# Optimization experiments

Measured on AMD Instinct MI355X. Metric: run time of the kernel, lower is better.

The kernel has to match this reference:

```python
import jax, jax.numpy as jnp
import numpy as np

WS = 7          # window size
DIM = 192
HEADS = 6
NW = 64         # number of windows per image (mask leading dim)
NC = 3          # n_contrast (q and kv)
B_ = 1024       # num_windows * batch


def _relative_position_index(ws):
    coords = np.stack(np.meshgrid(np.arange(ws), np.arange(ws), indexing='ij'))  # (2, ws, ws)
    cf = coords.reshape(2, -1)                       # (2, ws*ws)
    rel = cf[:, :, None] - cf[:, None, :]            # (2, N, N)
    rel = rel.transpose(1, 2, 0).copy()              # (N, N, 2)
    rel[:, :, 0] += ws - 1
    rel[:, :, 1] += ws - 1
    rel[:, :, 0] *= 2 * ws - 1
    return rel.sum(-1)                               # (N, N) int

REL_IDX = jnp.asarray(_relative_position_index(WS))


def setup_inputs() -> dict:
    key = jax.random.key(0)
    ks = jax.random.split(key, 13)
    f32 = jnp.float32
    inp = {
        'x_q': jax.random.normal(ks[0], (B_, NC, WS, WS, DIM), f32),
        'x_k': jax.random.normal(ks[1], (B_, NC, WS, WS, DIM), f32),
        'x_v': jax.random.normal(ks[2], (B_, NC, WS, WS, DIM), f32),
        'mask': jax.random.normal(ks[3], (NW, WS * WS, WS * WS), f32),
        # Linear weights stored torch-style: (out_features, in_features)
        'q_w': jax.random.normal(ks[4], (DIM, DIM), f32) * 0.02,
        'q_b': jnp.zeros((DIM,), f32),
        'k_w': jax.random.normal(ks[5], (DIM, DIM), f32) * 0.02,
        'k_b': jnp.zeros((DIM,), f32),
        'v_w': jax.random.normal(ks[6], (DIM, DIM), f32) * 0.02,
        'v_b': jnp.zeros((DIM,), f32),
        'proj_w': jax.random.normal(ks[7], (DIM, DIM), f32) * 0.02,
        'proj_b': jnp.zeros((DIM,), f32),
        'bias_table': jax.random.normal(ks[8], ((2 * WS - 1) ** 2, HEADS), f32) * 0.02,
    }
    return inp


def reference(x_q, x_k, x_v, mask, q_w, q_b, k_w, k_b, v_w, v_b, proj_w, proj_b, bias_table):
    Bw, ncq, Wh, Ww, C = x_q.shape
    nckv = x_k.shape[1]
    H = HEADS
    hd = C // H
    Nq = ncq * Wh * Ww
    Nkv = nckv * Wh * Ww

    xq = x_q.reshape(Bw, Nq, C)
    xk = x_k.reshape(Bw, Nkv, C)
    xv = x_v.reshape(Bw, Nkv, C)

    q = (xq @ q_w.T + q_b).reshape(Bw, Nq, H, hd).transpose(0, 2, 1, 3)   # (B_, H, Nq, hd)
    k = (xk @ k_w.T + k_b).reshape(Bw, Nkv, H, hd).transpose(0, 2, 1, 3)
    v = (xv @ v_w.T + v_b).reshape(Bw, Nkv, H, hd).transpose(0, 2, 1, 3)

    scale = hd ** (-0.5)
    attn = jnp.einsum('bhqd,bhkd->bhqk', q * scale, k)                    # (B_, H, Nq, Nkv)

    Nwin = Wh * Ww
    bias = bias_table[REL_IDX.reshape(-1)].reshape(Nwin, Nwin, H)
    bias = bias.transpose(2, 0, 1)                                        # (H, Nwin, Nwin)
    bias = jnp.tile(bias, (1, ncq, nckv))                                 # (H, Nq, Nkv)
    attn = attn + bias[None]

    nW = mask.shape[0]
    m = jnp.tile(mask, (1, ncq, nckv))                                    # (nW, Nq, Nkv)
    attn = attn.reshape(Bw // nW, nW, H, Nq, Nkv) + m[None, :, None]
    attn = attn.reshape(Bw, H, Nq, Nkv)
    attn = jax.nn.softmax(attn, axis=-1)

    out = jnp.einsum('bhqk,bhkd->bhqd', attn, v)                          # (B_, H, Nq, hd)
    out = out.transpose(0, 2, 1, 3).reshape(Bw, Nq, C)
    out = out @ proj_w.T + proj_b
    return out.reshape(Bw, ncq, Wh, Ww, C)
```

## Files before the change

### kernel.cpp

```cpp
#include <hip/hip_runtime.h>
#include <stdint.h>

#define ROWS 150528
#define QSCALE 0.17677669529663687f
#define L2E 1.44269504088896f

typedef __attribute__((ext_vector_type(8))) __bf16 bf16x8;
typedef __attribute__((ext_vector_type(4))) __bf16 bf16x4;
typedef __attribute__((ext_vector_type(4))) float f32x4;
typedef __attribute__((ext_vector_type(4))) float f4;
typedef __attribute__((ext_vector_type(2))) uint32_t u32x2;

static __device__ __forceinline__ f32x4 mfma_bf16(bf16x8 a, bf16x8 b, f32x4 c) {
  return __builtin_amdgcn_mfma_f32_16x16x32_bf16(a, b, c, 0, 0, 0);
}

static __device__ __forceinline__ uint32_t pack_bf16(float a, float b) {
  uint16_t ux = __builtin_bit_cast(uint16_t, (__bf16)a);
  uint16_t uy = __builtin_bit_cast(uint16_t, (__bf16)b);
  return (uint32_t)ux | ((uint32_t)uy << 16);
}

#define GLOAD_LDS16(gp, lp)                                                     \
  __builtin_amdgcn_global_load_lds(                                             \
      (const __attribute__((address_space(1))) uint32_t*)(gp),                  \
      (__attribute__((address_space(3))) uint32_t*)(lp), 16, 0, 0)

__global__ void prep(const float* __restrict__ q_w, const float* __restrict__ k_w,
                     const float* __restrict__ v_w, const float* __restrict__ p_w,
                     __bf16* __restrict__ wq, __bf16* __restrict__ wk,
                     __bf16* __restrict__ wv, __bf16* __restrict__ wp,
                     const float* __restrict__ maskp, const float* __restrict__ btab,
                     float* __restrict__ bmall) {
  const int bid = blockIdx.x;
  if (bid < 144) {
    const int y = bid / 36;
    const float* s = y == 0 ? q_w : y == 1 ? k_w : y == 2 ? v_w : p_w;
    __bf16* d = y == 0 ? wq : y == 1 ? wk : y == 2 ? wv : wp;
    int i = (bid % 36) * 256 + threadIdx.x;
    f4 v = ((const f4*)s)[i];
    bf16x4 b;
    b[0] = (__bf16)v[0]; b[1] = (__bf16)v[1]; b[2] = (__bf16)v[2]; b[3] = (__bf16)v[3];
    ((bf16x4*)d)[i] = b;
  } else {
    const int idx = bid - 144;
    const int win = idx / 6, h = idx - win * 6;
    float* dst = bmall + ((size_t)idx) * 2800;
    for (int i = threadIdx.x; i < 2796; i += 256) {
      int q = i / 57, ke = i - q * 57;
      int k = ke >= 49 ? ke - 49 : ke;
      if (q > 48) q = 48;
      int qi = q / 7, qj = q - qi * 7, ki = k / 7, kj = k - ki * 7;
      int rel = (qi - ki + 6) * 13 + (qj - kj + 6);
      dst[i] = (maskp[win * 2401 + q * 49 + k] + btab[rel * 6 + h]) * L2E;
    }
  }
}

template<bool IN_F32, bool OUT_F32, int RPT, int TILES>
static __device__ __forceinline__
void gemm_pipe(const void* __restrict__ Xv, const __bf16* __restrict__ Wb,
               const float* __restrict__ bias, void* __restrict__ Ov, float scale,
               char* Xs, int bx)
{
  constexpr int CPR = IN_F32 ? 48 : 24;
  constexpr int LPW = RPT * CPR / 256;
  constexpr int TB  = RPT * CPR * 16;
  constexpr int RG  = RPT / 16;
  constexpr int SPT = RG * 3;
  const int tid = threadIdx.x;
  const int wv = tid >> 6, lane = tid & 63, lr = lane & 15, lg = lane >> 4;
  const size_t blk0 = (size_t)bx * (RPT * TILES);

  bf16x8 wf[3][6];
  f4 bc4[3];
  #pragma unroll
  for (int t = 0; t < 3; ++t) {
    const int nt = wv + 4 * t;
    const __bf16* wr = &Wb[(nt * 16 + lr) * 192 + lg * 8];
    #pragma unroll
    for (int kk = 0; kk < 6; ++kk) wf[t][kk] = *(const bf16x8*)&wr[kk * 32];
    f4 bb = *(const f4*)&bias[nt * 16 + 4 * lg];
    #pragma unroll
    for (int e = 0; e < 4; ++e) bc4[t][e] = bb[e] * scale;
  }

  auto stage = [&](int buf, int t) {
    const size_t row0 = blk0 + (size_t)t * RPT;
    char* ldsb = Xs + buf * TB;
    int l = (wv * LPW) * 64 + lane;
    #pragma unroll
    for (int p = 0; p < LPW; ++p) {
      int r = l / CPR;
      int c16 = (l - r * CPR) ^ (r & 7);
      const char* src;
      if (IN_F32) {
        src = (const char*)Xv + ((row0 + r) * 768 + c16 * 16);
      } else {
        int hh = c16 >> 2, sub = c16 & 3;
        src = (const char*)Xv + (((size_t)hh * ROWS + row0 + r) * 64 + sub * 16);
      }
      GLOAD_LDS16(src, ldsb + (wv * LPW + p) * 1024);
      l += 64;
    }
  };

  stage(0, 0);
  stage(1, 1);

  #pragma unroll
  for (int it = 0; it < TILES; ++it) {
    if (it == 0) {
      asm volatile("s_waitcnt vmcnt(%0)" :: "i"(LPW) : "memory");
    } else if (it == 1) {
      asm volatile("s_waitcnt vmcnt(%0)" :: "i"(SPT + LPW) : "memory");
    } else if (it + 1 < TILES) {
      asm volatile("s_waitcnt vmcnt(%0)" :: "i"(2 * SPT + LPW) : "memory");
    } else {
      asm volatile("s_waitcnt vmcnt(%0)" :: "i"(2 * SPT) : "memory");
    }
    __builtin_amdgcn_s_barrier();

    const size_t row0 = blk0 + (size_t)it * RPT;
    const char* cb = Xs + (it % 3) * TB;

    bf16x8 a[RG][6];
    #pragma unroll
    for (int rg = 0; rg < RG; ++rg) {
      const int rr = rg * 16 + lr;
      const char* rb = cb + rr * (CPR * 16);
      const int sw = rr & 7;
      if (IN_F32) {
        #pragma unroll
        for (int kk = 0; kk < 6; ++kk) {
          const int g0 = kk * 8 + lg * 2;
          f4 lo = *(const f4*)(rb + ((g0 ^ sw) * 16));
          f4 hi = *(const f4*)(rb + (((g0 + 1) ^ sw) * 16));
          #pragma unroll
          for (int e = 0; e < 4; ++e) {
            a[rg][kk][e]     = (__bf16)lo[e];
            a[rg][kk][4 + e] = (__bf16)hi[e];
          }
        }
      } else {
        #pragma unroll
        for (int kk = 0; kk < 6; ++kk) {
          const int g = kk * 4 + lg;
          a[rg][kk] = *(const bf16x8*)(rb + ((g ^ sw) * 16));
        }
      }
    }

    if (it + 2 < TILES) stage((it + 2) % 3, it + 2);
    asm volatile("" ::: "memory");

    #pragma unroll
    for (int rg = 0; rg < RG; ++rg) {
      const size_t grow = row0 + rg * 16 + lr;
      #pragma unroll
      for (int t = 0; t < 3; ++t) {
        f32x4 acc = {0.f, 0.f, 0.f, 0.f};
        #pragma unroll
        for (int kk = 0; kk < 6; ++kk) acc = mfma_bf16(wf[t][kk], a[rg][kk], acc);
        const int nt = wv + 4 * t;
        if (OUT_F32) {
          f4 ov;
          #pragma unroll
          for (int j = 0; j < 4; ++j) ov[j] = acc[j] * scale + bc4[t][j];
          *(f4*)&((float*)Ov)[grow * 192 + nt * 16 + 4 * lg] = ov;
        } else {
          u32x2 pw;
          pw[0] = pack_bf16(acc[0] * scale + bc4[t][0], acc[1] * scale + bc4[t][1]);
          pw[1] = pack_bf16(acc[2] * scale + bc4[t][2], acc[3] * scale + bc4[t][3]);
          const int hh = nt >> 1;
          *(u32x2*)&((__bf16*)Ov)[((size_t)hh * ROWS + grow) * 32 +
                                  (nt & 1) * 16 + 4 * lg] = pw;
        }
      }
    }
    asm volatile("" ::: "memory");
  }
}

__global__ __launch_bounds__(256, 2)
void qkvgemm(const float* __restrict__ xq, const float* __restrict__ xk,
             const float* __restrict__ xv,
             const __bf16* __restrict__ wq, const __bf16* __restrict__ wk,
             const __bf16* __restrict__ wv,
             const float* __restrict__ bq, const float* __restrict__ bk,
             const float* __restrict__ bv,
             __bf16* __restrict__ oq, __bf16* __restrict__ ok,
             __bf16* __restrict__ ov)
{
  __shared__ __align__(16) char Xs[3 * 24576];
  const int y = blockIdx.y;
  const int bx = (blockIdx.x & 7) * 98 + (blockIdx.x >> 3);
  const float* x = y == 0 ? xq : y == 1 ? xk : xv;
  const __bf16* w = y == 0 ? wq : y == 1 ? wk : wv;
  const float* bi = y == 0 ? bq : y == 1 ? bk : bv;
  __bf16* o = y == 0 ? oq : y == 1 ? ok : ov;
  const float scale = y == 0 ? (QSCALE * L2E) : 1.f;
  gemm_pipe<true, false, 32, 6>(x, w, bi, o, scale, Xs, bx);
}

__global__ __launch_bounds__(256, 2)
void projgemm(const __bf16* __restrict__ X, const __bf16* __restrict__ Wb,
              const float* __restrict__ bias, float* __restrict__ Ov)
{
  __shared__ __align__(16) char Xs[3 * 12288];
  const int bx = (blockIdx.x & 7) * 98 + (blockIdx.x >> 3);
  gemm_pipe<false, true, 32, 6>(X, Wb, bias, Ov, 1.f, Xs, bx);
}

__global__ __launch_bounds__(320, 5)
void attn9(const __bf16* __restrict__ Q, const __bf16* __restrict__ K,
           const __bf16* __restrict__ V, __bf16* __restrict__ O,
           const float* __restrict__ bmall)
{
  __shared__ __align__(16) __bf16 Ks[160 * 40];
  __shared__ __align__(16) __bf16 Vt[32 * 168];
  __shared__ __align__(16) float bm2[2796];

  const int b = (blockIdx.x & 7) * 128 + (blockIdx.x >> 3);
  const int h = blockIdx.y;
  const int tid = threadIdx.x;
  const size_t hb = (size_t)h * ROWS + (size_t)b * 147;
  const int wv = tid >> 6, lane = tid & 63;
  const int lr = lane & 15, lg = lane >> 4;

  bf16x8 qf = *(const bf16x8*)&Q[(hb + wv * 16 + lr) * 32 + lg * 8];

  {
    const f4* bsrc = (const f4*)(bmall + (size_t)((b & 63) * 6 + h) * 2800);
    for (int i = tid; i < 699; i += 320) ((f4*)bm2)[i] = bsrc[i];
  }
  for (int i = tid; i < 588; i += 320) {
    int k = i >> 2, c = i & 3;
    int phys = (k & ~31) | (((k >> 2) & 1) << 4) | (((k >> 3) & 3) << 2) | (k & 3);
    *(bf16x8*)&Ks[phys * 40 + c * 8] = *(const bf16x8*)&K[(hb + k) * 32 + c * 8];
  }
  for (int t = tid; t < 588; t += 320) {
    int key = t >> 2, dblk = t & 3;
    bf16x8 v = *(const bf16x8*)&V[(hb + key) * 32 + dblk * 8];
    #pragma unroll
    for (int e = 0; e < 8; ++e) Vt[(dblk * 8 + e) * 168 + key] = v[e];
  }
  for (int i = tid; i < 32 * 13; i += 320) {
    int d = i / 13, key = 147 + (i - (i / 13) * 13);
    Vt[d * 168 + key] = (__bf16)0.f;
  }
  __syncthreads();

  #pragma unroll
  for (int t = 0; t < 2; ++t) {
    const int mt = wv + 5 * t;

    bf16x8 qn = qf;
    if (t == 0) {
      int qr = (wv + 5) * 16 + lr; if (qr > 146) qr = 146;
      qn = *(const bf16x8*)&Q[(hb + qr) * 32 + lg * 8];
    }

    int r = mt * 16 + lr;
    int q49 = r; if (q49 >= 98) q49 -= 98; if (q49 >= 49) q49 -= 49;
    const float* bmrow = &bm2[q49 * 57];

    f32x4 o0 = {0.f,0.f,0.f,0.f}, o1 = {0.f,0.f,0.f,0.f};
    float sum = 0.f;
    int kb = lg * 8;
    __builtin_amdgcn_s_setprio(1);
    #pragma unroll
    for (int s = 0; s < 5; ++s) {
      const f32x4 z = {0.f,0.f,0.f,0.f};
      f32x4 st0 = mfma_bf16(*(const bf16x8*)&Ks[(s * 32 + lr) * 40 + lg * 8], qf, z);
      f32x4 st1 = mfma_bf16(*(const bf16x8*)&Ks[(s * 32 + 16 + lr) * 40 + lg * 8], qf, z);
      const float* bp = bmrow + kb;
      #pragma unroll
      for (int j = 0; j < 4; ++j) { st0[j] += bp[j]; st1[j] += bp[4 + j]; }
      if (s == 4) {
        #pragma unroll
        for (int j = 0; j < 4; ++j) {
          if (lg * 8 + j >= 19) st0[j] = -1e30f;
          if (lg * 8 + j >= 15) st1[j] = -1e30f;
        }
      }
      #pragma unroll
      for (int j = 0; j < 4; ++j) { st0[j] = exp2f(st0[j]); sum += st0[j]; }
      #pragma unroll
      for (int j = 0; j < 4; ++j) { st1[j] = exp2f(st1[j]); sum += st1[j]; }
      union { bf16x8 v; uint32_t w[4]; } pu;
      pu.w[0] = pack_bf16(st0[0], st0[1]);
      pu.w[1] = pack_bf16(st0[2], st0[3]);
      pu.w[2] = pack_bf16(st1[0], st1[1]);
      pu.w[3] = pack_bf16(st1[2], st1[3]);
      bf16x8 v0 = *(const bf16x8*)&Vt[lr * 168 + s * 32 + lg * 8];
      bf16x8 v1 = *(const bf16x8*)&Vt[(16 + lr) * 168 + s * 32 + lg * 8];
      o0 = mfma_bf16(pu.v, v0, o0);
      o1 = mfma_bf16(pu.v, v1, o1);
      kb += 32; if (kb >= 49) kb -= 49;
    }
    __builtin_amdgcn_s_setprio(0);
    sum += __shfl_xor(sum, 16);
    sum += __shfl_xor(sum, 32);
    const float rinv = 1.f / sum;
    #pragma unroll
    for (int j = 0; j < 4; ++j) {
      const int qa = mt * 16 + lg * 4 + j;
      const float rj = __shfl(rinv, lg * 4 + j);
      if (qa < 147) {
        const size_t base = (hb + qa) * 32;
        O[base + lr]      = (__bf16)(o0[j] * rj);
        O[base + 16 + lr] = (__bf16)(o1[j] * rj);
      }
    }
    qf = qn;
  }
}

extern "C" void kernel_launch(void* const* d_in, const int* in_sizes, int n_in,
                              void* d_out, int out_size, void* d_ws, size_t ws_size,
                              hipStream_t stream) {
  (void)in_sizes; (void)n_in; (void)out_size;
  const float* x_q  = (const float*)d_in[0];
  const float* x_k  = (const float*)d_in[1];
  const float* x_v  = (const float*)d_in[2];
  const float* maskp= (const float*)d_in[3];
  const float* q_w  = (const float*)d_in[4];
  const float* q_b  = (const float*)d_in[5];
  const float* k_w  = (const float*)d_in[6];
  const float* k_b  = (const float*)d_in[7];
  const float* v_w  = (const float*)d_in[8];
  const float* v_b  = (const float*)d_in[9];
  const float* p_w  = (const float*)d_in[10];
  const float* p_b  = (const float*)d_in[11];
  const float* btab = (const float*)d_in[12];

  char* ws = (char*)d_ws;
  float* bmall = (float*)ws;
  const size_t bmsz = (size_t)64 * 6 * 2800 * sizeof(float);
  char* wsp = ws + bmsz;
  const size_t wsz = 36864 * sizeof(__bf16);
  __bf16* wq  = (__bf16*)wsp;
  __bf16* wk  = (__bf16*)(wsp + wsz);
  __bf16* wvp = (__bf16*)(wsp + 2 * wsz);
  __bf16* wp  = (__bf16*)(wsp + 3 * wsz);
  char* bufs = wsp + 4 * wsz;
  const size_t sz = (size_t)ROWS * 192 * sizeof(__bf16);
  __bf16* qb = (__bf16*)bufs;
  __bf16* kb = (__bf16*)(bufs + sz);
  __bf16* vb = (__bf16*)(bufs + 2 * sz);
  const size_t need4 = bmsz + 4 * wsz + 4 * sz;
  __bf16* ob = (ws_size >= need4) ? (__bf16*)(bufs + 3 * sz) : qb;

  prep<<<528, 256, 0, stream>>>(q_w, k_w, v_w, p_w, wq, wk, wvp, wp,
                                maskp, btab, bmall);

  qkvgemm<<<dim3(ROWS / 192, 3), 256, 0, stream>>>(x_q, x_k, x_v, wq, wk, wvp,
                                                   q_b, k_b, v_b, qb, kb, vb);

  attn9<<<dim3(1024, 6), 320, 0, stream>>>(qb, kb, vb, ob, bmall);

  projgemm<<<ROWS / 192, 256, 0, stream>>>(ob, wp, p_b, (float*)d_out);
}
```

Baseline: 265.5 us.

## Fold prep kernel into QKV GEMM and convert weights to bf16 in-register

Removes the separate prep launch. The GEMMs now read fp32 weights directly and convert them to bf16 in registers when loading the weight fragments. The mask-plus-bias table is built by 128 extra blocks appended to the QKV GEMM grid. The QKV GEMM tile also shrinks from 32 rows x 6 tiles to 16 rows x 8 tiles, with a smaller LDS buffer and a remapped block index. This saves one launch and a weight round trip, but each block now does redundant weight loads and conversions, and the aux blocks add tail imbalance.

```diff
diff --git a/kernel.cpp b/kernel.cpp
--- a/kernel.cpp
+++ b/kernel.cpp
@@ -26,40 +26,9 @@
       (const __attribute__((address_space(1))) uint32_t*)(gp),                  \
       (__attribute__((address_space(3))) uint32_t*)(lp), 16, 0, 0)
 
-__global__ void prep(const float* __restrict__ q_w, const float* __restrict__ k_w,
-                     const float* __restrict__ v_w, const float* __restrict__ p_w,
-                     __bf16* __restrict__ wq, __bf16* __restrict__ wk,
-                     __bf16* __restrict__ wv, __bf16* __restrict__ wp,
-                     const float* __restrict__ maskp, const float* __restrict__ btab,
-                     float* __restrict__ bmall) {
-  const int bid = blockIdx.x;
-  if (bid < 144) {
-    const int y = bid / 36;
-    const float* s = y == 0 ? q_w : y == 1 ? k_w : y == 2 ? v_w : p_w;
-    __bf16* d = y == 0 ? wq : y == 1 ? wk : y == 2 ? wv : wp;
-    int i = (bid % 36) * 256 + threadIdx.x;
-    f4 v = ((const f4*)s)[i];
-    bf16x4 b;
-    b[0] = (__bf16)v[0]; b[1] = (__bf16)v[1]; b[2] = (__bf16)v[2]; b[3] = (__bf16)v[3];
-    ((bf16x4*)d)[i] = b;
-  } else {
-    const int idx = bid - 144;
-    const int win = idx / 6, h = idx - win * 6;
-    float* dst = bmall + ((size_t)idx) * 2800;
-    for (int i = threadIdx.x; i < 2796; i += 256) {
-      int q = i / 57, ke = i - q * 57;
-      int k = ke >= 49 ? ke - 49 : ke;
-      if (q > 48) q = 48;
-      int qi = q / 7, qj = q - qi * 7, ki = k / 7, kj = k - ki * 7;
-      int rel = (qi - ki + 6) * 13 + (qj - kj + 6);
-      dst[i] = (maskp[win * 2401 + q * 49 + k] + btab[rel * 6 + h]) * L2E;
-    }
-  }
-}
-
 template<bool IN_F32, bool OUT_F32, int RPT, int TILES>
 static __device__ __forceinline__
-void gemm_pipe(const void* __restrict__ Xv, const __bf16* __restrict__ Wb,
+void gemm_pipe(const void* __restrict__ Xv, const float* __restrict__ Wf,
                const float* __restrict__ bias, void* __restrict__ Ov, float scale,
                char* Xs, int bx)
 {
@@ -77,9 +46,17 @@
   #pragma unroll
   for (int t = 0; t < 3; ++t) {
     const int nt = wv + 4 * t;
-    const __bf16* wr = &Wb[(nt * 16 + lr) * 192 + lg * 8];
-    #pragma unroll
-    for (int kk = 0; kk < 6; ++kk) wf[t][kk] = *(const bf16x8*)&wr[kk * 32];
+    const float* wr = &Wf[(nt * 16 + lr) * 192 + lg * 8];
+    #pragma unroll
+    for (int kk = 0; kk < 6; ++kk) {
+      f4 lo = *(const f4*)(wr + kk * 32);
+      f4 hi = *(const f4*)(wr + kk * 32 + 4);
+      #pragma unroll
+      for (int e = 0; e < 4; ++e) {
+        wf[t][kk][e]     = (__bf16)lo[e];
+        wf[t][kk][4 + e] = (__bf16)hi[e];
+      }
+    }
     f4 bb = *(const f4*)&bias[nt * 16 + 4 * lg];
     #pragma unroll
     for (int e = 0; e < 4; ++e) bc4[t][e] = bb[e] * scale;
@@ -185,31 +162,47 @@
 __global__ __launch_bounds__(256, 2)
 void qkvgemm(const float* __restrict__ xq, const float* __restrict__ xk,
              const float* __restrict__ xv,
-             const __bf16* __restrict__ wq, const __bf16* __restrict__ wk,
-             const __bf16* __restrict__ wv,
+             const float* __restrict__ q_w, const float* __restrict__ k_w,
+             const float* __restrict__ v_w,
              const float* __restrict__ bq, const float* __restrict__ bk,
              const float* __restrict__ bv,
              __bf16* __restrict__ oq, __bf16* __restrict__ ok,
-             __bf16* __restrict__ ov)
+             __bf16* __restrict__ ov,
+             const float* __restrict__ maskp, const float* __restrict__ btab,
+             float* __restrict__ bmall)
 {
-  __shared__ __align__(16) char Xs[3 * 24576];
+  __shared__ __align__(16) char Xs[3 * 12288];
   const int y = blockIdx.y;
-  const int bx = (blockIdx.x & 7) * 98 + (blockIdx.x >> 3);
+  if (blockIdx.x >= 1176) {
+    const int aux = (blockIdx.x - 1176) * 3 + y;
+    const int win = aux / 6, h = aux - win * 6;
+    float* dst = bmall + (size_t)aux * 2800;
+    for (int i = threadIdx.x; i < 2796; i += 256) {
+      int q = i / 57, ke = i - q * 57;
+      int k = ke >= 49 ? ke - 49 : ke;
+      if (q > 48) q = 48;
+      int qi = q / 7, qj = q - qi * 7, ki = k / 7, kj = k - ki * 7;
+      int rel = (qi - ki + 6) * 13 + (qj - kj + 6);
+      dst[i] = (maskp[win * 2401 + q * 49 + k] + btab[rel * 6 + h]) * L2E;
+    }
+    return;
+  }
+  const int bx = (blockIdx.x & 7) * 147 + (blockIdx.x >> 3);
   const float* x = y == 0 ? xq : y == 1 ? xk : xv;
-  const __bf16* w = y == 0 ? wq : y == 1 ? wk : wv;
+  const float* w = y == 0 ? q_w : y == 1 ? k_w : v_w;
   const float* bi = y == 0 ? bq : y == 1 ? bk : bv;
   __bf16* o = y == 0 ? oq : y == 1 ? ok : ov;
   const float scale = y == 0 ? (QSCALE * L2E) : 1.f;
-  gemm_pipe<true, false, 32, 6>(x, w, bi, o, scale, Xs, bx);
+  gemm_pipe<true, false, 16, 8>(x, w, bi, o, scale, Xs, bx);
 }
 
 __global__ __launch_bounds__(256, 2)
-void projgemm(const __bf16* __restrict__ X, const __bf16* __restrict__ Wb,
+void projgemm(const __bf16* __restrict__ X, const float* __restrict__ Wf,
               const float* __restrict__ bias, float* __restrict__ Ov)
 {
   __shared__ __align__(16) char Xs[3 * 12288];
   const int bx = (blockIdx.x & 7) * 98 + (blockIdx.x >> 3);
-  gemm_pipe<false, true, 32, 6>(X, Wb, bias, Ov, 1.f, Xs, bx);
+  gemm_pipe<false, true, 32, 6>(X, Wf, bias, Ov, 1.f, Xs, bx);
 }
 
 __global__ __launch_bounds__(320, 5)
@@ -338,27 +331,19 @@
   char* ws = (char*)d_ws;
   float* bmall = (float*)ws;
   const size_t bmsz = (size_t)64 * 6 * 2800 * sizeof(float);
-  char* wsp = ws + bmsz;
-  const size_t wsz = 36864 * sizeof(__bf16);
-  __bf16* wq  = (__bf16*)wsp;
-  __bf16* wk  = (__bf16*)(wsp + wsz);
-  __bf16* wvp = (__bf16*)(wsp + 2 * wsz);
-  __bf16* wp  = (__bf16*)(wsp + 3 * wsz);
-  char* bufs = wsp + 4 * wsz;
+  char* bufs = ws + bmsz;
   const size_t sz = (size_t)ROWS * 192 * sizeof(__bf16);
   __bf16* qb = (__bf16*)bufs;
   __bf16* kb = (__bf16*)(bufs + sz);
   __bf16* vb = (__bf16*)(bufs + 2 * sz);
-  const size_t need4 = bmsz + 4 * wsz + 4 * sz;
+  const size_t need4 = bmsz + 4 * sz;
   __bf16* ob = (ws_size >= need4) ? (__bf16*)(bufs + 3 * sz) : qb;
 
-  prep<<<528, 256, 0, stream>>>(q_w, k_w, v_w, p_w, wq, wk, wvp, wp,
-                                maskp, btab, bmall);
-
-  qkvgemm<<<dim3(ROWS / 192, 3), 256, 0, stream>>>(x_q, x_k, x_v, wq, wk, wvp,
-                                                   q_b, k_b, v_b, qb, kb, vb);
+  qkvgemm<<<dim3(1176 + 128, 3), 256, 0, stream>>>(
+      x_q, x_k, x_v, q_w, k_w, v_w, q_b, k_b, v_b, qb, kb, vb,
+      maskp, btab, bmall);
 
   attn9<<<dim3(1024, 6), 320, 0, stream>>>(qb, kb, vb, ob, bmall);
 
-  projgemm<<<ROWS / 192, 256, 0, stream>>>(ob, wp, p_b, (float*)d_out);
-}
+  projgemm<<<784, 256, 0, stream>>>(ob, p_w, p_b, (float*)d_out);
+}
```

New measurement: 290.9 us. 9.6% more time.
